# Kernel tuning notes

Hardware: AMD Instinct MI355X
Metric: run time of the kernel (lower is better)

Reference implementation:

```python
import jax, jax.numpy as jnp
import numpy as np

DEPTH = 16
PERCENT = 1.2
MAX_P = 5.0
# ps[t] = clip((t+1)*percent, 0, max_percent), as in the torch __init__
PS = np.clip((np.arange(DEPTH) + 1) * PERCENT, 0.0, MAX_P)


def setup_inputs() -> dict:
    key = jax.random.key(0)
    kx, kA = jax.random.split(key, 2)
    B, M, N = 16384, 256, 1024
    A = jax.random.normal(kA, (M, N), dtype=jnp.float32) / np.sqrt(M)
    # L = max eigenvalue of A^T A (as max_eig in the torch code), scaled by 1.001
    gram = np.asarray(A.T @ A)
    L = float(np.linalg.eigvalsh(gram)[-1]) * 1.001
    # init=True initialization: every bias layer weight is A.T / L, threshold = 1/L
    W = jnp.tile((A.T / L)[None, :, :], (DEPTH, 1, 1))  # [depth, N, M]
    threshold = jnp.ones((DEPTH,), dtype=jnp.float32) / L
    x = jax.random.normal(kx, (B, M), dtype=jnp.float32)
    return {"x": x, "A": A, "W": W, "threshold": threshold}


def _shrink(x, t):
    # soft threshold: sign(x) * max(|x| - t, 0)
    return jnp.sign(x) * jnp.maximum(jnp.abs(x) - t, 0.0)


def _shrinkss(x, t, p):
    # support-selection shrink: entries above both the learned threshold and the
    # per-row (100-p) percentile of |x| pass through untouched; the rest are
    # soft-thresholded. Mask and percentile are detached (no_grad in torch).
    n = x.shape[1]
    idx = int(np.ceil((100.0 - p) / 100.0 * n)) - 1  # static per iteration
    abs_x = jnp.abs(x)
    thresh = jax.lax.stop_gradient(jnp.sort(abs_x, axis=1)[:, idx])  # [B]
    mask = jax.lax.stop_gradient(
        ((abs_x >= t) & (abs_x >= thresh[:, None])).astype(x.dtype)
    )
    return mask * x + _shrink((1.0 - mask) * x, t)


def reference(x, A, W, threshold):
    # x: [B, M], A: [M, N], W: [depth, N, M], threshold: [depth]
    B = x.shape[0]
    N = A.shape[1]
    u = jnp.zeros((B, N), dtype=x.dtype)
    for i in range(DEPTH):
        r = x - u @ A.T                      # residual in measurement space [B, M]
        v = u + r @ W[i].T                   # gradient step via learned bias [B, N]
        u = _shrinkss(v, threshold[i], PS[i])
    return u
```

## Files before the change

### kernel.cpp

```cpp
#include <hip/hip_runtime.h>
#include <hip/hip_bf16.h>

#define B_ROWS 16384
#define M_DIM  256
#define N_DIM  1024
#define DEPTH  16

typedef __attribute__((ext_vector_type(8))) short short8;
typedef __attribute__((ext_vector_type(4))) float f32x4;
typedef __attribute__((ext_vector_type(2))) float f32x2;

#define ATP_OFF_B   0
#define WTP_OFF_B   1572864
#define RP_OFF_B    (1572864 + 25165824)
#define TAU_OFF_B   (RP_OFF_B + 25165824)
#define WS_FAST_NEED ((size_t)TAU_OFF_B + 65536)
#define WTP_SLICE   (64 * 8 * 3 * 512)
#define RP_PANEL_US 24576

#define AT_OFF 0
#define WT_OFF (262144)
#define WS_OLD_NEED ((size_t)(262144 + 16 * 262144) * 4)

__device__ __forceinline__ unsigned short bf16r(float f) {
    unsigned u = __float_as_uint(f);
    u += 0x7fffu + ((u >> 16) & 1u);
    return (unsigned short)(u >> 16);
}
__device__ __forceinline__ float bf2f(unsigned short h) {
    return __uint_as_float(((unsigned)h) << 16);
}
__device__ __forceinline__ void split3(float x, unsigned short& h, unsigned short& m,
                                       unsigned short& lo) {
    h = bf16r(x); float r1 = x - bf2f(h);
    m = bf16r(r1); float r2 = r1 - bf2f(m);
    lo = bf16r(r2);
}
__device__ __forceinline__ f32x4 MF(short8 a, short8 b, f32x4 c) {
    return __builtin_amdgcn_mfma_f32_16x16x32_bf16(a, b, c, 0, 0, 0);
}
__device__ __forceinline__ float shrink_one(float v, float t, float thrv) {
    float a = fabsf(v);
    return (a >= thrv) ? v : copysignf(fmaxf(a - t, 0.0f), v);
}

__global__ void prep_a_kernel(const float* __restrict__ A, unsigned short* __restrict__ ATp) {
    int g = blockIdx.x * 256 + threadIdx.x;
    if (g >= 16 * 32 * 64) return;
    int l = g & 63, kc = (g >> 6) & 31, tile = g >> 11;
    int row = tile * 16 + (l & 15);
    int k0 = kc * 32 + ((l >> 4) << 3);
    unsigned short h[8], m[8], lo[8];
#pragma unroll
    for (int j = 0; j < 8; ++j) split3(A[(size_t)row * N_DIM + k0 + j], h[j], m[j], lo[j]);
    size_t base = ((size_t)(tile * 32 + kc) * 3) * 512 + l * 8;
#pragma unroll
    for (int j = 0; j < 8; ++j) {
        ATp[base + j] = h[j];
        ATp[base + 512 + j] = m[j];
        ATp[base + 1024 + j] = lo[j];
    }
}

__global__ void prep_w_kernel(const float* __restrict__ W, unsigned short* __restrict__ WTp) {
    int g = blockIdx.x * 256 + threadIdx.x;
    if (g >= 16 * 64 * 8 * 64) return;
    int l = g & 63, kc = (g >> 6) & 7, tile = (g >> 9) & 63, it = g >> 15;
    int n = tile * 16 + (l & 15);
    int m0 = kc * 32 + ((l >> 4) << 3);
    const float* Wi = W + (size_t)it * N_DIM * M_DIM;
    unsigned short h[8], m[8], lo[8];
#pragma unroll
    for (int j = 0; j < 8; ++j) split3(Wi[(size_t)n * M_DIM + m0 + j], h[j], m[j], lo[j]);
    size_t base = (((size_t)(it * 64 + tile) * 8 + kc) * 3) * 512 + l * 8;
#pragma unroll
    for (int j = 0; j < 8; ++j) {
        WTp[base + j] = h[j];
        WTp[base + 512 + j] = m[j];
        WTp[base + 1024 + j] = lo[j];
    }
}

__global__ void prep_x_kernel(const float* __restrict__ x, unsigned short* __restrict__ RP) {
    int g = blockIdx.x * 256 + threadIdx.x;
    if (g >= 524288) return;
    int l = g & 63, kcp = (g >> 6) & 3, wm = (g >> 8) & 1, c = (g >> 9) & 1, panel = g >> 10;
    int row = panel * 32 + wm * 16 + (l & 15);
    int k0 = c * 128 + kcp * 32 + ((l >> 4) << 3);
    unsigned short h[8], m[8], lo[8];
#pragma unroll
    for (int j = 0; j < 8; ++j) split3(x[(size_t)row * M_DIM + k0 + j], h[j], m[j], lo[j]);
    size_t base = (size_t)panel * RP_PANEL_US + ((((c * 2 + wm) * 4 + kcp) * 3)) * 512 + l * 8;
#pragma unroll
    for (int j = 0; j < 8; ++j) {
        RP[base + j] = h[j];
        RP[base + 512 + j] = m[j];
        RP[base + 1024 + j] = lo[j];
    }
}

#define LSTR2 136

__global__ __launch_bounds__(1024)
void g1_kernel(const float* __restrict__ UV, const float* __restrict__ x,
               const unsigned short* __restrict__ ATp,
               const float* __restrict__ thr_all, const float* __restrict__ TAU,
               unsigned short* __restrict__ RP, int iter) {
    __align__(16) __shared__ unsigned short smem[24576];
    const int tid = threadIdx.x;
    const int l = tid & 63, w = tid >> 6;
    const int wm = w >> 3, wn = w & 7;
    const int panel = blockIdx.x;
    const int row0 = panel * 32;
    const int arow = 16 * wm + (l & 15);
    const int akl  = (l >> 4) << 3;
    const float tprev = thr_all[iter - 1];

    f32x4 acc_hi[2], acc_rest[2];
    double acc64[2][4];
#pragma unroll
    for (int t = 0; t < 2; ++t) {
        acc_hi[t] = (f32x4){0, 0, 0, 0};
        acc_rest[t] = (f32x4){0, 0, 0, 0};
#pragma unroll
        for (int e = 0; e < 4; ++e) acc64[t][e] = 0.0;
    }

    f32x2 st[2];
#pragma unroll
    for (int jj = 0; jj < 2; ++jj) {
        const int idx = tid + 1024 * jj;
        const int r = idx >> 6, kq = idx & 63;
        st[jj] = *(const f32x2*)&UV[(size_t)(row0 + r) * N_DIM + kq * 2];
    }

    for (int c = 0; c < 8; ++c) {
        __syncthreads();
#pragma unroll
        for (int jj = 0; jj < 2; ++jj) {
            const int idx = tid + 1024 * jj;
            const int r = idx >> 6, kq = idx & 63;
            const float thrv = fmaxf(tprev, TAU[row0 + r]);
            const float a0 = shrink_one(st[jj].x, tprev, thrv);
            const float a1 = shrink_one(st[jj].y, tprev, thrv);
            unsigned short h0, m0, lo0, h1, m1, lo1;
            split3(a0, h0, m0, lo0);
            split3(a1, h1, m1, lo1);
            const unsigned off = (unsigned)r * LSTR2 + kq * 2;
            *(unsigned*)&smem[off] = (unsigned)h0 | ((unsigned)h1 << 16);
            *(unsigned*)&smem[4352 + off] = (unsigned)m0 | ((unsigned)m1 << 16);
            *(unsigned*)&smem[8704 + off] = (unsigned)lo0 | ((unsigned)lo1 << 16);
        }
        __syncthreads();
        if (c < 7) {
#pragma unroll
            for (int jj = 0; jj < 2; ++jj) {
                const int idx = tid + 1024 * jj;
                const int r = idx >> 6, kq = idx & 63;
                st[jj] = *(const f32x2*)&UV[(size_t)(row0 + r) * N_DIM + (c + 1) * 128 + kq * 2];
            }
        }
#pragma unroll
        for (int kc = 0; kc < 4; ++kc) {
            const unsigned ao = (unsigned)arow * LSTR2 + kc * 32 + akl;
            short8 ah = *(const short8*)&smem[ao];
            short8 am = *(const short8*)&smem[4352 + ao];
            short8 al = *(const short8*)&smem[8704 + ao];
#pragma unroll
            for (int tt = 0; tt < 2; ++tt) {
                const int tile = wn * 2 + tt;
                const unsigned bo = ((unsigned)(tile * 32 + c * 4 + kc) * 3) * 512 + l * 8;
                short8 bh = *(const short8*)&ATp[bo];
                short8 bm = *(const short8*)&ATp[bo + 512];
                short8 bl = *(const short8*)&ATp[bo + 1024];
                acc_hi[tt] = MF(ah, bh, acc_hi[tt]);
                acc_rest[tt] = MF(ah, bm, acc_rest[tt]);
                acc_rest[tt] = MF(am, bh, acc_rest[tt]);
                acc_rest[tt] = MF(am, bm, acc_rest[tt]);
                acc_rest[tt] = MF(ah, bl, acc_rest[tt]);
                acc_rest[tt] = MF(al, bh, acc_rest[tt]);
            }
        }
#pragma unroll
        for (int tt = 0; tt < 2; ++tt) {
#pragma unroll
            for (int e = 0; e < 4; ++e) acc64[tt][e] += (double)acc_hi[tt][e];
            acc_hi[tt] = (f32x4){0, 0, 0, 0};
        }
    }

    __syncthreads();
    {
        const int cimg = wn >> 2, kcp = wn & 3;
        const unsigned fbase = ((((unsigned)(cimg * 2 + wm) * 4 + kcp) * 3)) * 512;
#pragma unroll
        for (int tt = 0; tt < 2; ++tt) {
            const int col = wn * 32 + tt * 16 + (l & 15);
            const int hi2 = (tt * 2 + ((l & 15) >> 3)) & 3;
#pragma unroll
            for (int e = 0; e < 4; ++e) {
                const int rl = ((l >> 4) << 2) + e;
                const int row = row0 + wm * 16 + rl;
                const double tot = acc64[tt][e] + (double)acc_rest[tt][e];
                const float rv = (float)((double)x[(size_t)row * M_DIM + col] - tot);
                unsigned short h, m, lo;
                split3(rv, h, m, lo);
                const unsigned sl = fbase + (unsigned)(hi2 * 16 + rl) * 8 + (l & 7);
                smem[sl] = h;
                smem[sl + 512] = m;
                smem[sl + 1024] = lo;
            }
        }
    }
    __syncthreads();
    {
        const uint4* s4 = (const uint4*)smem;
        uint4* d4 = (uint4*)(RP + (size_t)panel * RP_PANEL_US);
        d4[tid] = s4[tid];
        d4[tid + 1024] = s4[tid + 1024];
        d4[tid + 2048] = s4[tid + 2048];
    }
}

__global__ __launch_bounds__(1024)
void g2_kernel(const unsigned short* __restrict__ RP, const unsigned short* __restrict__ WTpi,
               const float* __restrict__ thr_all, const float* __restrict__ TAU,
               float* UV, int iter) {
    __align__(16) __shared__ unsigned short img[24576];
    const int tid = threadIdx.x;
    const int l = tid & 63, w = tid >> 6;
    const int wm = w >> 3, wn = w & 7;
    const int panel = blockIdx.x >> 2, cg = blockIdx.x & 3;
    const int row0 = panel * 32;

    {
        const uint4* s4 = (const uint4*)(RP + (size_t)panel * RP_PANEL_US);
        uint4* d4 = (uint4*)img;
        d4[tid] = s4[tid];
        d4[tid + 1024] = s4[tid + 1024];
        d4[tid + 2048] = s4[tid + 2048];
    }
    __syncthreads();

    f32x4 hi[2], rest[2], sum[2];
#pragma unroll
    for (int t = 0; t < 2; ++t) {
        hi[t] = (f32x4){0, 0, 0, 0};
        rest[t] = (f32x4){0, 0, 0, 0};
        sum[t] = (f32x4){0, 0, 0, 0};
    }

    for (int kc = 0; kc < 8; ++kc) {
        const unsigned ab = ((((unsigned)(kc >> 2) * 2 + wm) * 4 + (kc & 3)) * 3) * 512 + l * 8;
        short8 ah = *(const short8*)&img[ab];
        short8 am = *(const short8*)&img[ab + 512];
        short8 al = *(const short8*)&img[ab + 1024];
#pragma unroll
        for (int tt = 0; tt < 2; ++tt) {
            const int tile = cg * 16 + wn * 2 + tt;
            const unsigned bo = ((unsigned)(tile * 8 + kc) * 3) * 512 + l * 8;
            short8 bh = *(const short8*)&WTpi[bo];
            short8 bm = *(const short8*)&WTpi[bo + 512];
            short8 bl = *(const short8*)&WTpi[bo + 1024];
            hi[tt] = MF(ah, bh, hi[tt]);
            rest[tt] = MF(ah, bm, rest[tt]);
            rest[tt] = MF(am, bh, rest[tt]);
            rest[tt] = MF(am, bm, rest[tt]);
            rest[tt] = MF(ah, bl, rest[tt]);
            rest[tt] = MF(al, bh, rest[tt]);
        }
        if ((kc & 3) == 3) {
#pragma unroll
            for (int tt = 0; tt < 2; ++tt) {
#pragma unroll
                for (int e = 0; e < 4; ++e) sum[tt][e] += hi[tt][e];
                hi[tt] = (f32x4){0, 0, 0, 0};
            }
        }
    }

    const float tprev = (iter > 0) ? thr_all[iter - 1] : 0.0f;
#pragma unroll
    for (int tt = 0; tt < 2; ++tt) {
        const int col = cg * 256 + wn * 32 + tt * 16 + (l & 15);
#pragma unroll
        for (int e = 0; e < 4; ++e) {
            const int row = row0 + wm * 16 + ((l >> 4) << 2) + e;
            const float tot = sum[tt][e] + rest[tt][e];
            float us = 0.0f;
            if (iter > 0) {
                const float uo = UV[(size_t)row * N_DIM + col];
                const float thrv = fmaxf(tprev, TAU[row]);
                us = shrink_one(uo, tprev, thrv);
            }
            UV[(size_t)row * N_DIM + col] = us + tot;
        }
    }
}

__global__ __launch_bounds__(1024)
void stau_kernel(const float* __restrict__ UV, float* __restrict__ TAU, int kth) {
    const int lane = threadIdx.x & 63;
    const int wave = threadIdx.x >> 6;
    const int row = blockIdx.x * 16 + wave;
    const float* vp = UV + (size_t)row * N_DIM;
    unsigned key[16];
#pragma unroll
    for (int j = 0; j < 16; ++j)
        key[j] = __float_as_uint(vp[lane + 64 * j]) & 0x7fffffffu;
    unsigned p = 0;
#pragma unroll 1
    for (int b = 30; b >= 0; --b) {
        const unsigned cand = p | (1u << b);
        int cnt = 0;
#pragma unroll
        for (int j = 0; j < 16; ++j) cnt += (key[j] >= cand) ? 1 : 0;
#pragma unroll
        for (int off = 32; off; off >>= 1) cnt += __shfl_xor(cnt, off);
        if (cnt >= kth) p = cand;
    }
    if (lane == 0) TAU[row] = __uint_as_float(p);
}

__global__ __launch_bounds__(256)
void s_kernel(float* UV, const float* __restrict__ thr_all, int iter, int kth) {
    __shared__ float v_s[8][1024];
    __shared__ float tau_s[8];
    const int tid = threadIdx.x;
    const int lane = tid & 63;
    const int wave = tid >> 6;
    const int row0 = blockIdx.x * 8;
    const float t = thr_all[iter];
    {
        const float4* Vg4 = (const float4*)(UV + (size_t)row0 * N_DIM);
        float4* vs4 = (float4*)(&v_s[0][0]);
#pragma unroll
        for (int c = 0; c < 8; ++c) vs4[tid + 256 * c] = Vg4[tid + 256 * c];
    }
    __syncthreads();
#pragma unroll 1
    for (int rr = 0; rr < 2; ++rr) {
        const int row = wave + rr * 4;
        unsigned key[16];
#pragma unroll
        for (int j = 0; j < 16; ++j)
            key[j] = __float_as_uint(v_s[row][lane + 64 * j]) & 0x7fffffffu;
        unsigned p = 0;
#pragma unroll 1
        for (int b = 30; b >= 0; --b) {
            const unsigned cand = p | (1u << b);
            int cnt = 0;
#pragma unroll
            for (int j = 0; j < 16; ++j) cnt += (key[j] >= cand) ? 1 : 0;
#pragma unroll
            for (int off = 32; off; off >>= 1) cnt += __shfl_xor(cnt, off);
            if (cnt >= kth) p = cand;
        }
        if (lane == 0) tau_s[row] = __uint_as_float(p);
    }
    __syncthreads();
    {
        const float4* vs4 = (const float4*)&v_s[0][0];
        float4* Uw = (float4*)(UV + (size_t)row0 * N_DIM);
#pragma unroll 1
        for (int c = 0; c < 8; ++c) {
            const int idx = tid + 256 * c;
            const int row = idx >> 8;
            const float thrv = fmaxf(t, tau_s[row]);
            float4 v = vs4[idx];
            float4 o;
            o.x = shrink_one(v.x, t, thrv);
            o.y = shrink_one(v.y, t, thrv);
            o.z = shrink_one(v.z, t, thrv);
            o.w = shrink_one(v.w, t, thrv);
            Uw[idx] = o;
        }
    }
}

#define DFMA4(acc, s, v) do { \
    (acc).x += (double)(s) * (double)(v).x; \
    (acc).y += (double)(s) * (double)(v).y; \
    (acc).z += (double)(s) * (double)(v).z; \
    (acc).w += (double)(s) * (double)(v).w; } while (0)

__global__ void transpose_kernel(const float* __restrict__ in, float* __restrict__ out,
                                 int R, int C) {
    __shared__ float tile[32][33];
    int s = blockIdx.z;
    const float* ip = in + (size_t)s * R * C;
    float* op = out + (size_t)s * R * C;
    int c0 = blockIdx.x * 32, r0 = blockIdx.y * 32;
    int tx = threadIdx.x, ty = threadIdx.y;
#pragma unroll
    for (int k = 0; k < 4; ++k)
        tile[ty + 8 * k][tx] = ip[(size_t)(r0 + ty + 8 * k) * C + (c0 + tx)];
    __syncthreads();
#pragma unroll
    for (int k = 0; k < 4; ++k)
        op[(size_t)(c0 + ty + 8 * k) * R + (r0 + tx)] = tile[tx][ty + 8 * k];
}

__global__ void zero_kernel(float* __restrict__ p, int n) {
    int i = blockIdx.x * blockDim.x + threadIdx.x;
    int stride = gridDim.x * blockDim.x;
    for (; i < n; i += stride) p[i] = 0.0f;
}

template <bool T>
__device__ __forceinline__ float4 loadAT(const float* __restrict__ p, int n, int m4) {
    if constexpr (T) {
        return ((const float4*)p)[n * 64 + m4];
    } else {
        float4 r;
        r.x = p[(size_t)(4 * m4 + 0) * N_DIM + n];
        r.y = p[(size_t)(4 * m4 + 1) * N_DIM + n];
        r.z = p[(size_t)(4 * m4 + 2) * N_DIM + n];
        r.w = p[(size_t)(4 * m4 + 3) * N_DIM + n];
        return r;
    }
}
template <bool T>
__device__ __forceinline__ float4 loadWT(const float* __restrict__ p, int m, int n4) {
    if constexpr (T) {
        return ((const float4*)p)[m * 256 + n4];
    } else {
        float4 r;
        r.x = p[(size_t)(4 * n4 + 0) * M_DIM + m];
        r.y = p[(size_t)(4 * n4 + 1) * M_DIM + m];
        r.z = p[(size_t)(4 * n4 + 2) * M_DIM + m];
        r.w = p[(size_t)(4 * n4 + 3) * M_DIM + m];
        return r;
    }
}

template <bool T>
__global__ __launch_bounds__(256)
void lista_iter_kernel(const float* __restrict__ x, const float* __restrict__ Ap,
                       const float* __restrict__ Wp, const float* __restrict__ thr_all,
                       float* __restrict__ U, int iter, int kth) {
    __shared__ float u_s[8][1024];
    __shared__ float r_s[8][256];
    __shared__ float tau_s[8];
    const int tid = threadIdx.x;
    const int lane = tid & 63;
    const int wave = tid >> 6;
    const int row0 = blockIdx.x * 8;
    const float t = thr_all[iter];
    {
        const float4* Ug4 = (const float4*)(U + (size_t)row0 * N_DIM);
        float4* us4 = (float4*)(&u_s[0][0]);
#pragma unroll
        for (int c = 0; c < 8; ++c) us4[tid + 256 * c] = Ug4[tid + 256 * c];
    }
    __syncthreads();
    {
        double4 acc0 = {0, 0, 0, 0}, acc1 = {0, 0, 0, 0};
        const float4* u0p = (const float4*)&u_s[wave][0];
        const float4* u1p = (const float4*)&u_s[wave + 4][0];
        for (int n4 = 0; n4 < 256; ++n4) {
            float4 u0 = u0p[n4];
            float4 u1 = u1p[n4];
            float4 a0 = loadAT<T>(Ap, 4 * n4 + 0, lane);
            float4 a1 = loadAT<T>(Ap, 4 * n4 + 1, lane);
            float4 a2 = loadAT<T>(Ap, 4 * n4 + 2, lane);
            float4 a3 = loadAT<T>(Ap, 4 * n4 + 3, lane);
            DFMA4(acc0, u0.x, a0); DFMA4(acc0, u0.y, a1); DFMA4(acc0, u0.z, a2); DFMA4(acc0, u0.w, a3);
            DFMA4(acc1, u1.x, a0); DFMA4(acc1, u1.y, a1); DFMA4(acc1, u1.z, a2); DFMA4(acc1, u1.w, a3);
        }
        float4 xv0 = ((const float4*)(x + (size_t)(row0 + wave) * M_DIM))[lane];
        float4 xv1 = ((const float4*)(x + (size_t)(row0 + wave + 4) * M_DIM))[lane];
        float4 rv0, rv1;
        rv0.x = (float)((double)xv0.x - acc0.x);
        rv0.y = (float)((double)xv0.y - acc0.y);
        rv0.z = (float)((double)xv0.z - acc0.z);
        rv0.w = (float)((double)xv0.w - acc0.w);
        rv1.x = (float)((double)xv1.x - acc1.x);
        rv1.y = (float)((double)xv1.y - acc1.y);
        rv1.z = (float)((double)xv1.z - acc1.z);
        rv1.w = (float)((double)xv1.w - acc1.w);
        ((float4*)&r_s[wave][0])[lane] = rv0;
        ((float4*)&r_s[wave + 4][0])[lane] = rv1;
    }
    __syncthreads();
    {
        const float4* r0p = (const float4*)&r_s[wave][0];
        const float4* r1p = (const float4*)&r_s[wave + 4][0];
        float4* u0p = (float4*)&u_s[wave][0];
        float4* u1p = (float4*)&u_s[wave + 4][0];
#pragma unroll 1
        for (int q = 0; q < 4; ++q) {
            const int n4 = lane + 64 * q;
            double4 acc0 = {0, 0, 0, 0}, acc1 = {0, 0, 0, 0};
            for (int m4 = 0; m4 < 64; ++m4) {
                float4 r0 = r0p[m4];
                float4 r1 = r1p[m4];
                float4 w0 = loadWT<T>(Wp, 4 * m4 + 0, n4);
                float4 w1 = loadWT<T>(Wp, 4 * m4 + 1, n4);
                float4 w2 = loadWT<T>(Wp, 4 * m4 + 2, n4);
                float4 w3 = loadWT<T>(Wp, 4 * m4 + 3, n4);
                DFMA4(acc0, r0.x, w0); DFMA4(acc0, r0.y, w1); DFMA4(acc0, r0.z, w2); DFMA4(acc0, r0.w, w3);
                DFMA4(acc1, r1.x, w0); DFMA4(acc1, r1.y, w1); DFMA4(acc1, r1.z, w2); DFMA4(acc1, r1.w, w3);
            }
            float4 uv0 = u0p[n4];
            uv0.x = (float)((double)uv0.x + acc0.x);
            uv0.y = (float)((double)uv0.y + acc0.y);
            uv0.z = (float)((double)uv0.z + acc0.z);
            uv0.w = (float)((double)uv0.w + acc0.w);
            u0p[n4] = uv0;
            float4 uv1 = u1p[n4];
            uv1.x = (float)((double)uv1.x + acc1.x);
            uv1.y = (float)((double)uv1.y + acc1.y);
            uv1.z = (float)((double)uv1.z + acc1.z);
            uv1.w = (float)((double)uv1.w + acc1.w);
            u1p[n4] = uv1;
        }
    }
    __syncthreads();
    {
#pragma unroll 1
        for (int rr = 0; rr < 2; ++rr) {
            const int row = wave + rr * 4;
            unsigned key[16];
#pragma unroll
            for (int j = 0; j < 16; ++j)
                key[j] = __float_as_uint(u_s[row][lane + 64 * j]) & 0x7fffffffu;
            unsigned p = 0;
#pragma unroll 1
            for (int b = 30; b >= 0; --b) {
                const unsigned cand = p | (1u << b);
                int cnt = 0;
#pragma unroll
                for (int j = 0; j < 16; ++j) cnt += (key[j] >= cand) ? 1 : 0;
#pragma unroll
                for (int off = 32; off; off >>= 1) cnt += __shfl_xor(cnt, off);
                if (cnt >= kth) p = cand;
            }
            if (lane == 0) tau_s[row] = __uint_as_float(p);
        }
    }
    __syncthreads();
    {
        const float4* us4 = (const float4*)&u_s[0][0];
        float4* Uw = (float4*)(U + (size_t)row0 * N_DIM);
#pragma unroll 1
        for (int c = 0; c < 8; ++c) {
            const int idx = tid + 256 * c;
            const int row = idx >> 8;
            const float thrv = fmaxf(t, tau_s[row]);
            float4 v = us4[idx];
            float4 o;
            o.x = shrink_one(v.x, t, thrv);
            o.y = shrink_one(v.y, t, thrv);
            o.z = shrink_one(v.z, t, thrv);
            o.w = shrink_one(v.w, t, thrv);
            Uw[idx] = o;
        }
    }
}

extern "C" void kernel_launch(void* const* d_in, const int* in_sizes, int n_in,
                              void* d_out, int out_size, void* d_ws, size_t ws_size,
                              hipStream_t stream) {
    const float* x   = (const float*)d_in[0];
    const float* A   = (const float*)d_in[1];
    const float* W   = (const float*)d_in[2];
    const float* thr = (const float*)d_in[3];

    float* UV = (float*)d_out;

    static const int ktab[DEPTH] = {13, 25, 37, 50, 52, 52, 52, 52,
                                    52, 52, 52, 52, 52, 52, 52, 52};

    if (ws_size >= WS_FAST_NEED) {
        unsigned short* ATp = (unsigned short*)((char*)d_ws + ATP_OFF_B);
        unsigned short* WTp = (unsigned short*)((char*)d_ws + WTP_OFF_B);
        unsigned short* RP  = (unsigned short*)((char*)d_ws + RP_OFF_B);
        float* TAU = (float*)((char*)d_ws + TAU_OFF_B);

        prep_a_kernel<<<128, 256, 0, stream>>>(A, ATp);
        prep_w_kernel<<<2048, 256, 0, stream>>>(W, WTp);
        prep_x_kernel<<<2048, 256, 0, stream>>>(x, RP);

        g2_kernel<<<2048, 1024, 0, stream>>>(RP, WTp, thr, TAU, UV, 0);
        stau_kernel<<<B_ROWS / 16, 1024, 0, stream>>>(UV, TAU, ktab[0]);

        for (int it = 1; it < DEPTH; ++it) {
            g1_kernel<<<512, 1024, 0, stream>>>(UV, x, ATp, thr, TAU, RP, it);
            g2_kernel<<<2048, 1024, 0, stream>>>(RP, WTp + (size_t)it * WTP_SLICE,
                                                 thr, TAU, UV, it);
            if (it < DEPTH - 1)
                stau_kernel<<<B_ROWS / 16, 1024, 0, stream>>>(UV, TAU, ktab[it]);
            else
                s_kernel<<<B_ROWS / 8, 256, 0, stream>>>(UV, thr, it, ktab[it]);
        }
    } else if (ws_size >= WS_OLD_NEED) {
        float* ws = (float*)d_ws;
        float* AT = ws + AT_OFF;
        float* WT = ws + WT_OFF;
        zero_kernel<<<1024, 256, 0, stream>>>(UV, B_ROWS * N_DIM);
        dim3 tb(32, 8);
        transpose_kernel<<<dim3(N_DIM / 32, M_DIM / 32, 1), tb, 0, stream>>>(A, AT, M_DIM, N_DIM);
        transpose_kernel<<<dim3(M_DIM / 32, N_DIM / 32, DEPTH), tb, 0, stream>>>(W, WT, N_DIM, M_DIM);
        for (int it = 0; it < DEPTH; ++it)
            lista_iter_kernel<true><<<B_ROWS / 8, 256, 0, stream>>>(
                x, AT, WT + (size_t)it * M_DIM * N_DIM, thr, UV, it, ktab[it]);
    } else {
        zero_kernel<<<1024, 256, 0, stream>>>(UV, B_ROWS * N_DIM);
        for (int it = 0; it < DEPTH; ++it)
            lista_iter_kernel<false><<<B_ROWS / 8, 256, 0, stream>>>(
                x, A, W + (size_t)it * N_DIM * M_DIM, thr, UV, it, ktab[it]);
    }
}
```

Baseline: 3.172 ms.

## Halve block size, widen per-wave tiles, double-buffer g1 LDS, drop g2 LDS staging

Both GEMM kernels drop from 1024 to 512 threads, and each wave now computes four 16-column tiles instead of two, so every A fragment load is reused across more MFMAs. g1 double-buffers its shared-memory chunk and prefetches UV two chunks ahead, which removes one barrier per chunk iteration. g2 no longer copies the RP panel into LDS and reads A fragments straight from global memory. The trade-off is higher register pressure from the larger accumulator and double arrays, plus reliance on cache hits for the now-uncached A reads in g2.

```diff
diff --git a/kernel.cpp b/kernel.cpp
--- a/kernel.cpp
+++ b/kernel.cpp
@@ -100,75 +100,93 @@
 }
 
 #define LSTR2 136
-
-__global__ __launch_bounds__(1024)
+#define BUFUS 13056
+
+__global__ __launch_bounds__(512)
 void g1_kernel(const float* __restrict__ UV, const float* __restrict__ x,
                const unsigned short* __restrict__ ATp,
                const float* __restrict__ thr_all, const float* __restrict__ TAU,
                unsigned short* __restrict__ RP, int iter) {
-    __align__(16) __shared__ unsigned short smem[24576];
+    __align__(16) __shared__ unsigned short smem[2 * BUFUS];
     const int tid = threadIdx.x;
     const int l = tid & 63, w = tid >> 6;
-    const int wm = w >> 3, wn = w & 7;
+    const int wm = w >> 2, wn = w & 3;
     const int panel = blockIdx.x;
     const int row0 = panel * 32;
     const int arow = 16 * wm + (l & 15);
     const int akl  = (l >> 4) << 3;
     const float tprev = thr_all[iter - 1];
 
-    f32x4 acc_hi[2], acc_rest[2];
-    double acc64[2][4];
-#pragma unroll
-    for (int t = 0; t < 2; ++t) {
+    f32x4 acc_hi[4], acc_rest[4];
+    double acc64[4][4];
+#pragma unroll
+    for (int t = 0; t < 4; ++t) {
         acc_hi[t] = (f32x4){0, 0, 0, 0};
         acc_rest[t] = (f32x4){0, 0, 0, 0};
 #pragma unroll
         for (int e = 0; e < 4; ++e) acc64[t][e] = 0.0;
     }
 
-    f32x2 st[2];
-#pragma unroll
-    for (int jj = 0; jj < 2; ++jj) {
-        const int idx = tid + 1024 * jj;
-        const int r = idx >> 6, kq = idx & 63;
-        st[jj] = *(const f32x2*)&UV[(size_t)(row0 + r) * N_DIM + kq * 2];
-    }
-
-    for (int c = 0; c < 8; ++c) {
-        __syncthreads();
-#pragma unroll
-        for (int jj = 0; jj < 2; ++jj) {
-            const int idx = tid + 1024 * jj;
-            const int r = idx >> 6, kq = idx & 63;
-            const float thrv = fmaxf(tprev, TAU[row0 + r]);
-            const float a0 = shrink_one(st[jj].x, tprev, thrv);
-            const float a1 = shrink_one(st[jj].y, tprev, thrv);
+    int srow[4]; unsigned soff[4]; float thrv_r[4]; const float* uvp[4];
+#pragma unroll
+    for (int jj = 0; jj < 4; ++jj) {
+        const int idx = tid + 512 * jj;
+        srow[jj] = idx >> 6;
+        const int kq = idx & 63;
+        soff[jj] = (unsigned)srow[jj] * LSTR2 + kq * 2;
+        thrv_r[jj] = fmaxf(tprev, TAU[row0 + srow[jj]]);
+        uvp[jj] = UV + (size_t)(row0 + srow[jj]) * N_DIM + kq * 2;
+    }
+
+    f32x2 st[4];
+#pragma unroll
+    for (int jj = 0; jj < 4; ++jj) st[jj] = *(const f32x2*)(uvp[jj]);
+    {
+#pragma unroll
+        for (int jj = 0; jj < 4; ++jj) {
+            const float a0 = shrink_one(st[jj].x, tprev, thrv_r[jj]);
+            const float a1 = shrink_one(st[jj].y, tprev, thrv_r[jj]);
             unsigned short h0, m0, lo0, h1, m1, lo1;
             split3(a0, h0, m0, lo0);
             split3(a1, h1, m1, lo1);
-            const unsigned off = (unsigned)r * LSTR2 + kq * 2;
-            *(unsigned*)&smem[off] = (unsigned)h0 | ((unsigned)h1 << 16);
-            *(unsigned*)&smem[4352 + off] = (unsigned)m0 | ((unsigned)m1 << 16);
-            *(unsigned*)&smem[8704 + off] = (unsigned)lo0 | ((unsigned)lo1 << 16);
-        }
-        __syncthreads();
+            *(unsigned*)&smem[soff[jj]] = (unsigned)h0 | ((unsigned)h1 << 16);
+            *(unsigned*)&smem[4352 + soff[jj]] = (unsigned)m0 | ((unsigned)m1 << 16);
+            *(unsigned*)&smem[8704 + soff[jj]] = (unsigned)lo0 | ((unsigned)lo1 << 16);
+        }
+    }
+#pragma unroll
+    for (int jj = 0; jj < 4; ++jj) st[jj] = *(const f32x2*)(uvp[jj] + 128);
+    __syncthreads();
+
+    for (int c = 0; c < 8; ++c) {
+        const unsigned bb = (unsigned)(c & 1) * BUFUS;
+        const unsigned nb = (unsigned)((c + 1) & 1) * BUFUS;
         if (c < 7) {
 #pragma unroll
-            for (int jj = 0; jj < 2; ++jj) {
-                const int idx = tid + 1024 * jj;
-                const int r = idx >> 6, kq = idx & 63;
-                st[jj] = *(const f32x2*)&UV[(size_t)(row0 + r) * N_DIM + (c + 1) * 128 + kq * 2];
+            for (int jj = 0; jj < 4; ++jj) {
+                const float a0 = shrink_one(st[jj].x, tprev, thrv_r[jj]);
+                const float a1 = shrink_one(st[jj].y, tprev, thrv_r[jj]);
+                unsigned short h0, m0, lo0, h1, m1, lo1;
+                split3(a0, h0, m0, lo0);
+                split3(a1, h1, m1, lo1);
+                *(unsigned*)&smem[nb + soff[jj]] = (unsigned)h0 | ((unsigned)h1 << 16);
+                *(unsigned*)&smem[nb + 4352 + soff[jj]] = (unsigned)m0 | ((unsigned)m1 << 16);
+                *(unsigned*)&smem[nb + 8704 + soff[jj]] = (unsigned)lo0 | ((unsigned)lo1 << 16);
             }
         }
+        if (c < 6) {
+#pragma unroll
+            for (int jj = 0; jj < 4; ++jj) st[jj] = *(const f32x2*)(uvp[jj] + (c + 2) * 128);
+        }
 #pragma unroll
         for (int kc = 0; kc < 4; ++kc) {
-            const unsigned ao = (unsigned)arow * LSTR2 + kc * 32 + akl;
+            const unsigned ao = bb + (unsigned)arow * LSTR2 + kc * 32 + akl;
             short8 ah = *(const short8*)&smem[ao];
-            short8 am = *(const short8*)&smem[4352 + ao];
-            short8 al = *(const short8*)&smem[8704 + ao];
-#pragma unroll
-            for (int tt = 0; tt < 2; ++tt) {
-                const int tile = wn * 2 + tt;
+            short8 am = *(const short8*)&smem[ao + 4352];
+            short8 al = *(const short8*)&smem[ao + 8704];
+#pragma unroll
+            for (int tt = 0; tt < 4; ++tt) {
+                const int tile = wn * 4 + tt;
                 const unsigned bo = ((unsigned)(tile * 32 + c * 4 + kc) * 3) * 512 + l * 8;
                 short8 bh = *(const short8*)&ATp[bo];
                 short8 bm = *(const short8*)&ATp[bo + 512];
@@ -182,21 +200,22 @@
             }
         }
 #pragma unroll
-        for (int tt = 0; tt < 2; ++tt) {
+        for (int tt = 0; tt < 4; ++tt) {
 #pragma unroll
             for (int e = 0; e < 4; ++e) acc64[tt][e] += (double)acc_hi[tt][e];
             acc_hi[tt] = (f32x4){0, 0, 0, 0};
         }
-    }
-
-    __syncthreads();
-    {
-        const int cimg = wn >> 2, kcp = wn & 3;
-        const unsigned fbase = ((((unsigned)(cimg * 2 + wm) * 4 + kcp) * 3)) * 512;
-#pragma unroll
-        for (int tt = 0; tt < 2; ++tt) {
-            const int col = wn * 32 + tt * 16 + (l & 15);
-            const int hi2 = (tt * 2 + ((l & 15) >> 3)) & 3;
+        __syncthreads();
+    }
+
+    {
+#pragma unroll
+        for (int tt = 0; tt < 4; ++tt) {
+            const int col = wn * 64 + tt * 16 + (l & 15);
+            const unsigned cimg = (unsigned)col >> 7;
+            const unsigned kcp = ((unsigned)col >> 5) & 3;
+            const unsigned hi2 = ((unsigned)col >> 3) & 3;
+            const unsigned fbase = (((cimg * 2 + wm) * 4 + kcp) * 3) * 512;
 #pragma unroll
             for (int e = 0; e < 4; ++e) {
                 const int rl = ((l >> 4) << 2) + e;
@@ -216,35 +235,25 @@
     {
         const uint4* s4 = (const uint4*)smem;
         uint4* d4 = (uint4*)(RP + (size_t)panel * RP_PANEL_US);
-        d4[tid] = s4[tid];
-        d4[tid + 1024] = s4[tid + 1024];
-        d4[tid + 2048] = s4[tid + 2048];
-    }
-}
-
-__global__ __launch_bounds__(1024)
+#pragma unroll
+        for (int q = 0; q < 6; ++q) d4[tid + 512 * q] = s4[tid + 512 * q];
+    }
+}
+
+__global__ __launch_bounds__(512)
 void g2_kernel(const unsigned short* __restrict__ RP, const unsigned short* __restrict__ WTpi,
                const float* __restrict__ thr_all, const float* __restrict__ TAU,
                float* UV, int iter) {
-    __align__(16) __shared__ unsigned short img[24576];
     const int tid = threadIdx.x;
     const int l = tid & 63, w = tid >> 6;
-    const int wm = w >> 3, wn = w & 7;
+    const int wm = w >> 2, wn = w & 3;
     const int panel = blockIdx.x >> 2, cg = blockIdx.x & 3;
     const int row0 = panel * 32;
-
-    {
-        const uint4* s4 = (const uint4*)(RP + (size_t)panel * RP_PANEL_US);
-        uint4* d4 = (uint4*)img;
-        d4[tid] = s4[tid];
-        d4[tid + 1024] = s4[tid + 1024];
-        d4[tid + 2048] = s4[tid + 2048];
-    }
-    __syncthreads();
-
-    f32x4 hi[2], rest[2], sum[2];
-#pragma unroll
-    for (int t = 0; t < 2; ++t) {
+    const unsigned short* Ap = RP + (size_t)panel * RP_PANEL_US;
+
+    f32x4 hi[4], rest[4], sum[4];
+#pragma unroll
+    for (int t = 0; t < 4; ++t) {
         hi[t] = (f32x4){0, 0, 0, 0};
         rest[t] = (f32x4){0, 0, 0, 0};
         sum[t] = (f32x4){0, 0, 0, 0};
@@ -252,12 +261,12 @@
 
     for (int kc = 0; kc < 8; ++kc) {
         const unsigned ab = ((((unsigned)(kc >> 2) * 2 + wm) * 4 + (kc & 3)) * 3) * 512 + l * 8;
-        short8 ah = *(const short8*)&img[ab];
-        short8 am = *(const short8*)&img[ab + 512];
-        short8 al = *(const short8*)&img[ab + 1024];
-#pragma unroll
-        for (int tt = 0; tt < 2; ++tt) {
-            const int tile = cg * 16 + wn * 2 + tt;
+        short8 ah = *(const short8*)&Ap[ab];
+        short8 am = *(const short8*)&Ap[ab + 512];
+        short8 al = *(const short8*)&Ap[ab + 1024];
+#pragma unroll
+        for (int tt = 0; tt < 4; ++tt) {
+            const int tile = cg * 16 + wn * 4 + tt;
             const unsigned bo = ((unsigned)(tile * 8 + kc) * 3) * 512 + l * 8;
             short8 bh = *(const short8*)&WTpi[bo];
             short8 bm = *(const short8*)&WTpi[bo + 512];
@@ -271,7 +280,7 @@
         }
         if ((kc & 3) == 3) {
 #pragma unroll
-            for (int tt = 0; tt < 2; ++tt) {
+            for (int tt = 0; tt < 4; ++tt) {
 #pragma unroll
                 for (int e = 0; e < 4; ++e) sum[tt][e] += hi[tt][e];
                 hi[tt] = (f32x4){0, 0, 0, 0};
@@ -281,8 +290,8 @@
 
     const float tprev = (iter > 0) ? thr_all[iter - 1] : 0.0f;
 #pragma unroll
-    for (int tt = 0; tt < 2; ++tt) {
-        const int col = cg * 256 + wn * 32 + tt * 16 + (l & 15);
+    for (int tt = 0; tt < 4; ++tt) {
+        const int col = cg * 256 + wn * 64 + tt * 16 + (l & 15);
 #pragma unroll
         for (int e = 0; e < 4; ++e) {
             const int row = row0 + wm * 16 + ((l >> 4) << 2) + e;
@@ -582,13 +591,13 @@
         prep_w_kernel<<<2048, 256, 0, stream>>>(W, WTp);
         prep_x_kernel<<<2048, 256, 0, stream>>>(x, RP);
 
-        g2_kernel<<<2048, 1024, 0, stream>>>(RP, WTp, thr, TAU, UV, 0);
+        g2_kernel<<<2048, 512, 0, stream>>>(RP, WTp, thr, TAU, UV, 0);
         stau_kernel<<<B_ROWS / 16, 1024, 0, stream>>>(UV, TAU, ktab[0]);
 
         for (int it = 1; it < DEPTH; ++it) {
-            g1_kernel<<<512, 1024, 0, stream>>>(UV, x, ATp, thr, TAU, RP, it);
-            g2_kernel<<<2048, 1024, 0, stream>>>(RP, WTp + (size_t)it * WTP_SLICE,
-                                                 thr, TAU, UV, it);
+            g1_kernel<<<512, 512, 0, stream>>>(UV, x, ATp, thr, TAU, RP, it);
+            g2_kernel<<<2048, 512, 0, stream>>>(RP, WTp + (size_t)it * WTP_SLICE,
+                                                thr, TAU, UV, it);
             if (it < DEPTH - 1)
                 stau_kernel<<<B_ROWS / 16, 1024, 0, stream>>>(UV, TAU, ktab[it]);
             else
```

After: 3.553 ms. +12.0%, slower.

## Fuse per-row percentile threshold search into g1 and double-buffer LDS staging

Applied to the files above, without the earlier changes.

Removes the separate stau_kernel launch by computing each row's percentile threshold with the bitwise radix search inside g1_kernel, keeping it in shared memory and also writing it to TAU for g2. The shrink/split staging of UV chunks into LDS is also double-buffered, so each chunk needs one barrier instead of two. This saves a launch and a full UV read pass per iteration, but g1 now reads each UV row twice and runs a serial 31-step search before its matmul starts. LDS use grows to two buffers.

```diff
diff --git a/kernel.cpp b/kernel.cpp
--- a/kernel.cpp
+++ b/kernel.cpp
@@ -100,13 +100,15 @@
 }
 
 #define LSTR2 136
+#define BUFUS 13056
 
 __global__ __launch_bounds__(1024)
 void g1_kernel(const float* __restrict__ UV, const float* __restrict__ x,
                const unsigned short* __restrict__ ATp,
-               const float* __restrict__ thr_all, const float* __restrict__ TAU,
-               unsigned short* __restrict__ RP, int iter) {
-    __align__(16) __shared__ unsigned short smem[24576];
+               const float* __restrict__ thr_all, float* __restrict__ TAU,
+               unsigned short* __restrict__ RP, int iter, int kth_prev) {
+    __align__(16) __shared__ unsigned short smem[2 * BUFUS];
+    __shared__ float tau_s[32];
     const int tid = threadIdx.x;
     const int l = tid & 63, w = tid >> 6;
     const int wm = w >> 3, wn = w & 7;
@@ -116,6 +118,34 @@
     const int akl  = (l >> 4) << 3;
     const float tprev = thr_all[iter - 1];
 
+    {
+#pragma unroll 1
+        for (int rr = 0; rr < 2; ++rr) {
+            const int row = w * 2 + rr;
+            const float* vp = UV + (size_t)(row0 + row) * N_DIM;
+            unsigned key[16];
+#pragma unroll
+            for (int j = 0; j < 16; ++j)
+                key[j] = __float_as_uint(vp[l + 64 * j]) & 0x7fffffffu;
+            unsigned p = 0;
+#pragma unroll 1
+            for (int b = 30; b >= 0; --b) {
+                const unsigned cand = p | (1u << b);
+                int cnt = 0;
+#pragma unroll
+                for (int j = 0; j < 16; ++j) cnt += (key[j] >= cand) ? 1 : 0;
+#pragma unroll
+                for (int off = 32; off; off >>= 1) cnt += __shfl_xor(cnt, off);
+                if (cnt >= kth_prev) p = cand;
+            }
+            if (l == 0) {
+                tau_s[row] = __uint_as_float(p);
+                TAU[row0 + row] = __uint_as_float(p);
+            }
+        }
+    }
+    __syncthreads();
+
     f32x4 acc_hi[2], acc_rest[2];
     double acc64[2][4];
 #pragma unroll
@@ -133,39 +163,63 @@
         const int r = idx >> 6, kq = idx & 63;
         st[jj] = *(const f32x2*)&UV[(size_t)(row0 + r) * N_DIM + kq * 2];
     }
+#pragma unroll
+    for (int jj = 0; jj < 2; ++jj) {
+        const int idx = tid + 1024 * jj;
+        const int r = idx >> 6, kq = idx & 63;
+        const float thrv = fmaxf(tprev, tau_s[r]);
+        const float a0 = shrink_one(st[jj].x, tprev, thrv);
+        const float a1 = shrink_one(st[jj].y, tprev, thrv);
+        unsigned short h0, m0, lo0, h1, m1, lo1;
+        split3(a0, h0, m0, lo0);
+        split3(a1, h1, m1, lo1);
+        const unsigned off = (unsigned)r * LSTR2 + kq * 2;
+        *(unsigned*)&smem[off] = (unsigned)h0 | ((unsigned)h1 << 16);
+        *(unsigned*)&smem[4352 + off] = (unsigned)m0 | ((unsigned)m1 << 16);
+        *(unsigned*)&smem[8704 + off] = (unsigned)lo0 | ((unsigned)lo1 << 16);
+    }
+#pragma unroll
+    for (int jj = 0; jj < 2; ++jj) {
+        const int idx = tid + 1024 * jj;
+        const int r = idx >> 6, kq = idx & 63;
+        st[jj] = *(const f32x2*)&UV[(size_t)(row0 + r) * N_DIM + 128 + kq * 2];
+    }
+    __syncthreads();
 
     for (int c = 0; c < 8; ++c) {
-        __syncthreads();
-#pragma unroll
-        for (int jj = 0; jj < 2; ++jj) {
-            const int idx = tid + 1024 * jj;
-            const int r = idx >> 6, kq = idx & 63;
-            const float thrv = fmaxf(tprev, TAU[row0 + r]);
-            const float a0 = shrink_one(st[jj].x, tprev, thrv);
-            const float a1 = shrink_one(st[jj].y, tprev, thrv);
-            unsigned short h0, m0, lo0, h1, m1, lo1;
-            split3(a0, h0, m0, lo0);
-            split3(a1, h1, m1, lo1);
-            const unsigned off = (unsigned)r * LSTR2 + kq * 2;
-            *(unsigned*)&smem[off] = (unsigned)h0 | ((unsigned)h1 << 16);
-            *(unsigned*)&smem[4352 + off] = (unsigned)m0 | ((unsigned)m1 << 16);
-            *(unsigned*)&smem[8704 + off] = (unsigned)lo0 | ((unsigned)lo1 << 16);
-        }
-        __syncthreads();
+        const unsigned bb = (unsigned)(c & 1) * BUFUS;
+        const unsigned nb = (unsigned)((c + 1) & 1) * BUFUS;
         if (c < 7) {
 #pragma unroll
             for (int jj = 0; jj < 2; ++jj) {
                 const int idx = tid + 1024 * jj;
                 const int r = idx >> 6, kq = idx & 63;
-                st[jj] = *(const f32x2*)&UV[(size_t)(row0 + r) * N_DIM + (c + 1) * 128 + kq * 2];
+                const float thrv = fmaxf(tprev, tau_s[r]);
+                const float a0 = shrink_one(st[jj].x, tprev, thrv);
+                const float a1 = shrink_one(st[jj].y, tprev, thrv);
+                unsigned short h0, m0, lo0, h1, m1, lo1;
+                split3(a0, h0, m0, lo0);
+                split3(a1, h1, m1, lo1);
+                const unsigned off = (unsigned)r * LSTR2 + kq * 2;
+                *(unsigned*)&smem[nb + off] = (unsigned)h0 | ((unsigned)h1 << 16);
+                *(unsigned*)&smem[nb + 4352 + off] = (unsigned)m0 | ((unsigned)m1 << 16);
+                *(unsigned*)&smem[nb + 8704 + off] = (unsigned)lo0 | ((unsigned)lo1 << 16);
+            }
+        }
+        if (c < 6) {
+#pragma unroll
+            for (int jj = 0; jj < 2; ++jj) {
+                const int idx = tid + 1024 * jj;
+                const int r = idx >> 6, kq = idx & 63;
+                st[jj] = *(const f32x2*)&UV[(size_t)(row0 + r) * N_DIM + (c + 2) * 128 + kq * 2];
             }
         }
 #pragma unroll
         for (int kc = 0; kc < 4; ++kc) {
-            const unsigned ao = (unsigned)arow * LSTR2 + kc * 32 + akl;
+            const unsigned ao = bb + (unsigned)arow * LSTR2 + kc * 32 + akl;
             short8 ah = *(const short8*)&smem[ao];
-            short8 am = *(const short8*)&smem[4352 + ao];
-            short8 al = *(const short8*)&smem[8704 + ao];
+            short8 am = *(const short8*)&smem[ao + 4352];
+            short8 al = *(const short8*)&smem[ao + 8704];
 #pragma unroll
             for (int tt = 0; tt < 2; ++tt) {
                 const int tile = wn * 2 + tt;
@@ -187,9 +241,9 @@
             for (int e = 0; e < 4; ++e) acc64[tt][e] += (double)acc_hi[tt][e];
             acc_hi[tt] = (f32x4){0, 0, 0, 0};
         }
-    }
-
-    __syncthreads();
+        __syncthreads();
+    }
+
     {
         const int cimg = wn >> 2, kcp = wn & 3;
         const unsigned fbase = ((((unsigned)(cimg * 2 + wm) * 4 + kcp) * 3)) * 512;
@@ -296,30 +350,6 @@
             UV[(size_t)row * N_DIM + col] = us + tot;
         }
     }
-}
-
-__global__ __launch_bounds__(1024)
-void stau_kernel(const float* __restrict__ UV, float* __restrict__ TAU, int kth) {
-    const int lane = threadIdx.x & 63;
-    const int wave = threadIdx.x >> 6;
-    const int row = blockIdx.x * 16 + wave;
-    const float* vp = UV + (size_t)row * N_DIM;
-    unsigned key[16];
-#pragma unroll
-    for (int j = 0; j < 16; ++j)
-        key[j] = __float_as_uint(vp[lane + 64 * j]) & 0x7fffffffu;
-    unsigned p = 0;
-#pragma unroll 1
-    for (int b = 30; b >= 0; --b) {
-        const unsigned cand = p | (1u << b);
-        int cnt = 0;
-#pragma unroll
-        for (int j = 0; j < 16; ++j) cnt += (key[j] >= cand) ? 1 : 0;
-#pragma unroll
-        for (int off = 32; off; off >>= 1) cnt += __shfl_xor(cnt, off);
-        if (cnt >= kth) p = cand;
-    }
-    if (lane == 0) TAU[row] = __uint_as_float(p);
 }
 
 __global__ __launch_bounds__(256)
@@ -583,17 +613,14 @@
         prep_x_kernel<<<2048, 256, 0, stream>>>(x, RP);
 
         g2_kernel<<<2048, 1024, 0, stream>>>(RP, WTp, thr, TAU, UV, 0);
-        stau_kernel<<<B_ROWS / 16, 1024, 0, stream>>>(UV, TAU, ktab[0]);
 
         for (int it = 1; it < DEPTH; ++it) {
-            g1_kernel<<<512, 1024, 0, stream>>>(UV, x, ATp, thr, TAU, RP, it);
+            g1_kernel<<<512, 1024, 0, stream>>>(UV, x, ATp, thr, TAU, RP, it,
+                                                ktab[it - 1]);
             g2_kernel<<<2048, 1024, 0, stream>>>(RP, WTp + (size_t)it * WTP_SLICE,
                                                  thr, TAU, UV, it);
-            if (it < DEPTH - 1)
-                stau_kernel<<<B_ROWS / 16, 1024, 0, stream>>>(UV, TAU, ktab[it]);
-            else
-                s_kernel<<<B_ROWS / 8, 256, 0, stream>>>(UV, thr, it, ktab[it]);
-        }
+        }
+        s_kernel<<<B_ROWS / 8, 256, 0, stream>>>(UV, thr, DEPTH - 1, ktab[DEPTH - 1]);
     } else if (ws_size >= WS_OLD_NEED) {
         float* ws = (float*)d_ws;
         float* AT = ws + AT_OFF;
```

New measurement: 3.182 ms. Within noise of the previous version (+0.3%).
